# Optimization experiments

Hardware: AMD Instinct MI355X
Metric: run time of the kernel (lower is better)

## Reference

```python
import jax, jax.numpy as jnp
import numpy as np

BS, N, FIN = 128, 320, 1
H1, F1 = 8, 18   # layer-1 heads / hidden
H2, F2 = 4, 46   # layer-2 heads / hidden
D1 = H1 * F1     # 144
D2 = H2 * F2     # 184
FC = (104, 45, 84)
ALPHA = 0.2
NEG = -9e15


def _xavier(key, shape):
    fan_in, fan_out = shape[-2], shape[-1]
    s = 1.414 * np.sqrt(2.0 / (fan_in + fan_out))
    return jax.random.normal(key, shape, dtype=jnp.float32) * s


def setup_inputs() -> dict:
    key = jax.random.key(0)
    ks = jax.random.split(key, 20)
    xnodes = jax.random.normal(ks[0], (BS, N, FIN), dtype=jnp.float32)
    adj = (jax.random.uniform(ks[1], (N, N)) < 0.1).astype(jnp.float32)
    adj = jnp.maximum(adj, jnp.eye(N, dtype=jnp.float32))
    inp = {
        'xnodes': xnodes,
        'adj': adj,
        'W1': _xavier(ks[2], (H1, FIN, F1)),
        'a1': _xavier(ks[3], (H1, 2 * F1)),
        'W2': _xavier(ks[4], (H2, D1, F2)),
        'a2': _xavier(ks[5], (H2, 2 * F2)),
        'p1w': _xavier(ks[6], (D1, 1))[:, 0],
        'p1b': jnp.zeros((), jnp.float32),
        'p2w': _xavier(ks[7], (D2, 1))[:, 0],
        'p2b': jnp.zeros((), jnp.float32),
        'e1w': _xavier(ks[8], (3 * N, FC[0])),
        'e1b': jnp.zeros((FC[0],), jnp.float32),
        'e2w': _xavier(ks[9], (FC[0], FC[1])),
        'e2b': jnp.zeros((FC[1],), jnp.float32),
        'e3w': _xavier(ks[10], (FC[1], FC[2])),
        'e3b': jnp.zeros((FC[2],), jnp.float32),
        'cw': _xavier(ks[11], (FC[2], 1))[:, 0],
        'cb': jnp.zeros((), jnp.float32),
    }
    return inp


def _gat(x, adj_mask, W, a):
    """Multi-head GAT layer (all heads vectorized).
    x: [b,n,fin], W: [h,fin,f], a: [h,2f], adj_mask: [n,n] bool.
    Score e_ij = leakyrelu(a_src.h_i + a_dst.h_j) == concat-matmul of the
    original, without materializing the [b,n,n,2f] tensor.
    """
    h = jnp.einsum('bni,hif->bhnf', x, W)              # [b,h,n,f]
    f = h.shape[-1]
    es = jnp.einsum('bhnf,hf->bhn', h, a[:, :f])       # source term
    ed = jnp.einsum('bhnf,hf->bhn', h, a[:, f:])       # dest term
    e = jax.nn.leaky_relu(es[:, :, :, None] + ed[:, :, None, :], ALPHA)
    e = jnp.where(adj_mask[None, None], e, NEG)
    att = jax.nn.softmax(e, axis=-1)                   # [b,h,n,n]
    hp = jnp.einsum('bhnm,bhmf->bhnf', att, h)
    out = jax.nn.elu(hp)                               # concat=True
    b = out.shape[0]
    return out.transpose(0, 2, 1, 3).reshape(b, out.shape[2], -1)  # [b,n,h*f]


def reference(xnodes, adj, W1, a1, W2, a2, p1w, p1b, p2w, p2b,
              e1w, e1b, e2w, e2b, e3w, e3b, cw, cb):
    mask = adj > 0
    x0 = jnp.mean(xnodes, axis=-1)                     # [b,n]
    x = _gat(xnodes, mask, W1, a1)                     # [b,n,144]
    x1 = x @ p1w + p1b                                 # pool1 -> [b,n]
    x = _gat(x, mask, W2, a2)                          # [b,n,184]
    x2 = x @ p2w + p2b                                 # pool2 -> [b,n]
    x_concat = jnp.concatenate([x0, x1, x2], axis=1)   # [b,3n]
    h = jax.nn.elu(x_concat @ e1w + e1b)
    h = jax.nn.elu(h @ e2w + e2b)
    features = jax.nn.elu(h @ e3w + e3b)               # [b,84]
    hazard = (features @ cw + cb).reshape(-1)          # [b]
    return (x_concat, features, hazard)
```

## Files before the change

### kernel.cpp

```cpp
#include <hip/hip_runtime.h>
#include <hip/hip_bf16.h>
#include <math.h>

#define BS 128
#define NN 320
#define H1 8
#define F1 18
#define H2C 4
#define F2 46
#define FC0 104
#define FC1 45
#define FC2 84
#define LRA 0.2f
#define DEGCAP 96
#define PW 104

typedef __attribute__((ext_vector_type(8))) short bf16x8;
typedef __attribute__((ext_vector_type(4))) float f32x4;

__device__ __forceinline__ float wave_max64(float v) {
    #pragma unroll
    for (int off = 32; off > 0; off >>= 1)
        v = fmaxf(v, __shfl_xor(v, off, 64));
    return v;
}
__device__ __forceinline__ short bfb(float x) {
    __hip_bfloat16 b = __float2bfloat16(x);
    return *(short*)&b;
}

__global__ void k_csr(const float* __restrict__ adj,
                      unsigned short* __restrict__ cols16,
                      unsigned short* __restrict__ colsT16,
                      int4* __restrict__ meta, const float* __restrict__ W1,
                      const float* __restrict__ a1, float* __restrict__ c1s,
                      float* __restrict__ c1d, const float* __restrict__ W2,
                      __hip_bfloat16* __restrict__ Bb) {
    int row = blockIdx.x;
    int lane = threadIdx.x;
    if (row < NN) {
        int base = 0, c96 = 0, c192 = 0, c288 = 0;
        for (int c0 = 0; c0 < NN; c0 += 64) {
            int j = c0 + lane;
            bool p = (j < NN) && (adj[row * NN + j] > 0.f);
            unsigned long long m = __ballot(p);
            if (p) {
                int pos = base + __popcll(m & ((1ull << lane) - 1ull));
                if (pos < DEGCAP) {
                    cols16[row * DEGCAP + pos] = (unsigned short)j;
                    colsT16[pos * NN + row] = (unsigned short)j;
                }
            }
            base += __popcll(m);
            c96  += __popcll(__ballot(p && j < 96));
            c192 += __popcll(__ballot(p && j < 192));
            c288 += __popcll(__ballot(p && j < 288));
        }
        if (base > DEGCAP) base = DEGCAP;
        if (c96 > DEGCAP) c96 = DEGCAP;
        if (c192 > DEGCAP) c192 = DEGCAP;
        if (c288 > DEGCAP) c288 = DEGCAP;
        for (int q = base + lane; q < DEGCAP; q += 64) {
            cols16[row * DEGCAP + q] = 0;
            colsT16[q * NN + row] = 0;
        }
        if (lane == 0) meta[row] = make_int4(c96, c192, c288, base);
    } else if (row == NN) {
        int h = lane;
        if (h < H1) {
            float s = 0.f, d = 0.f;
            for (int f = 0; f < F1; ++f) {
                float w = W1[h * F1 + f];
                s += w * a1[h * 2 * F1 + f];
                d += w * a1[h * 2 * F1 + F1 + f];
            }
            c1s[h] = s;
            c1d[h] = d;
        }
    } else {
        int idx = (row - NN - 1) * 64 + lane;
        int e = idx & 7;
        int t = idx >> 3;
        int n = t % 192, k8 = t / 192;
        int k = k8 * 8 + e, hh = n / 48, f = n - hh * 48;
        float v = (k < 144 && f < 46) ? W2[(hh * 144 + k) * 46 + f] : 0.f;
        Bb[idx] = __float2bfloat16(v);
    }
}

__global__ __launch_bounds__(320) void k_l1(
    const float* __restrict__ xn, const unsigned short* __restrict__ colsT16,
    const int4* __restrict__ meta, const float* __restrict__ W1,
    const float* __restrict__ c1s, const float* __restrict__ c1d,
    const float* __restrict__ p1w, float* __restrict__ sg,
    float* __restrict__ part1) {
    int b = blockIdx.x >> 3, h = blockIdx.x & 7;
    __shared__ float xb[NN];
    __shared__ float w1h[F1], pwl[F1];
    __shared__ float redmax[5], redmin[5];
    int tid = threadIdx.x;
    int wv = tid >> 6, lane = tid & 63;
    float xi = xn[b * NN + tid];
    xb[tid] = xi;
    if (tid < F1) { w1h[tid] = W1[h * F1 + tid]; pwl[tid] = p1w[h * F1 + tid]; }
    int Li = meta[tid].w;
    float mx = wave_max64(xi);
    float mn = -wave_max64(-xi);
    int Lmax = (int)wave_max64((float)Li);
    if (lane == 0) { redmax[wv] = mx; redmin[wv] = mn; }
    __syncthreads();
    float MX = redmax[0], MN = redmin[0];
    #pragma unroll
    for (int q = 1; q < 5; ++q) {
        MX = fmaxf(MX, redmax[q]);
        MN = fminf(MN, redmin[q]);
    }
    float cs = c1s[h], cd = c1d[h];
    float u = xi * cs;
    float mt = u + (cd > 0.f ? cd * MX : cd * MN);
    float m = fmaxf(mt, LRA * mt);
    float num = 0.f, den = 0.f;
    const unsigned short* ct = colsT16 + tid;
    int colv = ct[0];
    for (int j = 0; j < Lmax; ++j) {
        int coln = (j + 1 < Lmax) ? ct[(j + 1) * NN] : 0;
        float xj = xb[colv];
        bool act = j < Li;
        float t = fmaf(xj, cd, u);
        t = fmaxf(t, LRA * t);
        float w = __expf(t - m);
        w = act ? w : 0.f;
        num = fmaf(w, xj, num);
        den += w;
        colv = coln;
    }
    float s = num / den;
    sg[(size_t)(b * 8 + h) * NN + tid] = s;
    float part = 0.f;
    #pragma unroll
    for (int f = 0; f < F1; ++f) {
        float v = s * w1h[f];
        v = v > 0.f ? v : expm1f(v);
        part = fmaf(v, pwl[f], part);
    }
    part1[(size_t)(b * 8 + h) * NN + tid] = part;
}

__global__ __launch_bounds__(256) void k_l2(
    const float* __restrict__ sg, const unsigned short* __restrict__ cols16,
    const int4* __restrict__ meta, const __hip_bfloat16* __restrict__ Bb,
    const float* __restrict__ W1, const float* __restrict__ a2,
    const float* __restrict__ p2w, float* __restrict__ part2) {
    int bh = blockIdx.x;
    int b = bh >> 2, h = bh & 3;
    __shared__ __align__(16) __hip_bfloat16 HT[48][328];
    __shared__ __align__(16) __hip_bfloat16 AsP[4][16][PW];
    __shared__ __align__(16) unsigned short colsW[4][16][DEGCAP];
    __shared__ float sglW[4][8][16];
    __shared__ float esl[NN], edl[NN];
    __shared__ float denW[4][16];
    __shared__ float w1l[8][F1];
    __shared__ float pwl[48], a2e[48], a2d[48];
    __shared__ float Mred[4];
    int tid = threadIdx.x, wv = tid >> 6, lane = tid & 63;
    int lr = lane & 15, lq = lane >> 4;
    if (tid < 48) {
        pwl[tid] = tid < 46 ? p2w[h * F2 + tid] : 0.f;
        a2e[tid] = tid < 46 ? a2[h * 92 + tid] : 0.f;
        a2d[tid] = tid < 46 ? a2[h * 92 + 46 + tid] : 0.f;
    }
    if (tid < 144) {
        int hh = tid / F1, f = tid - hh * F1;
        w1l[hh][f] = W1[hh * F1 + f];
    }
    bf16x8 bq[5][3];
    #pragma unroll
    for (int kc = 0; kc < 5; ++kc)
        #pragma unroll
        for (int t = 0; t < 3; ++t)
            bq[kc][t] = *(const bf16x8*)(Bb +
                (size_t)(((kc * 4 + lq) * 192) + h * 48 + t * 16 + lr) * 8);
    __syncthreads();
    for (int tile = 0; tile < 5; ++tile) {
        int r0 = tile * 64;
        for (int q = lane; q < 128; q += 64) {
            int hh = q >> 4, row = q & 15;
            sglW[wv][hh][row] = sg[(size_t)(b * 8 + hh) * NN + r0 + wv * 16 + row];
        }
        f32x4 acc[3];
        #pragma unroll
        for (int t = 0; t < 3; ++t) acc[t] = (f32x4){0.f, 0.f, 0.f, 0.f};
        #pragma unroll
        for (int sp = 0; sp < 2; ++sp) {
            const int nch = sp ? 2 : 3;
            #pragma unroll
            for (int j = 0; j < nch; ++j) {
                int chunk = (sp ? 12 : 0) + lq + 4 * j;
                int cb = chunk * 8;
                bf16x8 pv;
                #pragma unroll
                for (int e = 0; e < 8; ++e) {
                    unsigned c = cb + e;
                    float v = 0.f;
                    if (c < 144) {
                        unsigned hh = c / 18, f = c - hh * 18;
                        v = sglW[wv][hh][lr] * w1l[hh][f];
                        v = v > 0.f ? v : expm1f(v);
                    }
                    pv[e] = bfb(v);
                }
                *(bf16x8*)&AsP[wv][lr][cb - sp * 96] = pv;
            }
            const int nkc = sp ? 2 : 3;
            #pragma unroll
            for (int kc2 = 0; kc2 < nkc; ++kc2) {
                bf16x8 a = *(const bf16x8*)&AsP[wv][lr][kc2 * 32 + lq * 8];
                int gkc = sp ? 3 + kc2 : kc2;
                #pragma unroll
                for (int t = 0; t < 3; ++t)
                    acc[t] = __builtin_amdgcn_mfma_f32_16x16x32_bf16(
                        a, bq[gkc][t], acc[t], 0, 0, 0);
            }
        }
        int node = r0 + wv * 16 + lq * 4;
        #pragma unroll
        for (int t = 0; t < 3; ++t) {
            short4 s4;
            s4.x = bfb(acc[t][0]); s4.y = bfb(acc[t][1]);
            s4.z = bfb(acc[t][2]); s4.w = bfb(acc[t][3]);
            *(short4*)&HT[t * 16 + lr][node] = s4;
        }
        float esa[4] = {0.f, 0.f, 0.f, 0.f}, eda[4] = {0.f, 0.f, 0.f, 0.f};
        #pragma unroll
        for (int t = 0; t < 3; ++t) {
            float ae = a2e[t * 16 + lr], ad = a2d[t * 16 + lr];
            #pragma unroll
            for (int j = 0; j < 4; ++j) {
                esa[j] = fmaf(acc[t][j], ae, esa[j]);
                eda[j] = fmaf(acc[t][j], ad, eda[j]);
            }
        }
        #pragma unroll
        for (int j = 0; j < 4; ++j) {
            #pragma unroll
            for (int off = 1; off < 16; off <<= 1) {
                esa[j] += __shfl_xor(esa[j], off, 64);
                eda[j] += __shfl_xor(eda[j], off, 64);
            }
        }
        if (lr == 0) {
            #pragma unroll
            for (int j = 0; j < 4; ++j) {
                esl[node + j] = esa[j];
                edl[node + j] = eda[j];
            }
        }
    }
    __syncthreads();
    float edmax = -1e30f;
    for (int i = tid; i < NN; i += 256) edmax = fmaxf(edmax, edl[i]);
    float wm = wave_max64(edmax);
    if (lane == 0) Mred[wv] = wm;
    __syncthreads();
    float M = fmaxf(fmaxf(Mred[0], Mred[1]), fmaxf(Mred[2], Mred[3]));
    for (int tile = 0; tile < 5; ++tile) {
        int r0 = tile * 64;
        for (int q = lane; q < 192; q += 64) {
            int rr = q / 12, c8 = q - rr * 12;
            *(uint4*)&colsW[wv][rr][c8 * 8] =
                *(const uint4*)(cols16 + (size_t)(r0 + wv * 16 + rr) * DEGCAP + c8 * 8);
        }
        int i = r0 + wv * 16 + lr;
        int4 mt = meta[i];
        int sb0 = mt.x, sb1 = mt.y, sb2 = mt.z, sb3 = mt.w;
        float es = esl[i];
        float t0 = es + M;
        float m = fmaxf(t0, LRA * t0);
        f32x4 acc[3];
        #pragma unroll
        for (int t = 0; t < 3; ++t) acc[t] = (f32x4){0.f, 0.f, 0.f, 0.f};
        float dp = 0.f;
        #pragma unroll
        for (int pass = 0; pass < 4; ++pass) {
            for (int q = lane; q < 208; q += 64) {
                int rr = q / 13, cc = q - rr * 13;
                *(uint4*)&AsP[wv][rr][cc * 8] = (uint4){0u, 0u, 0u, 0u};
            }
            int s0 = pass == 0 ? 0 : (pass == 1 ? sb0 : (pass == 2 ? sb1 : sb2));
            int s1 = pass == 0 ? sb0 : (pass == 1 ? sb1 : (pass == 2 ? sb2 : sb3));
            int pofs = pass * 96;
            for (int j = s0 + lq; j < s1; j += 4) {
                int col = colsW[wv][lr][j];
                float t = es + edl[col];
                t = fmaxf(t, LRA * t);
                float w = __expf(t - m);
                dp += w;
                AsP[wv][lr][col - pofs] = __float2bfloat16(w);
            }
            const int nkf = (pass < 3) ? 3 : 1;
            #pragma unroll
            for (int kf = 0; kf < nkf; ++kf) {
                bf16x8 a = *(const bf16x8*)&AsP[wv][lr][kf * 32 + lq * 8];
                #pragma unroll
                for (int t = 0; t < 3; ++t) {
                    bf16x8 bb = *(const bf16x8*)&HT[t * 16 + lr][pofs + kf * 32 + lq * 8];
                    acc[t] = __builtin_amdgcn_mfma_f32_16x16x32_bf16(
                        a, bb, acc[t], 0, 0, 0);
                }
            }
        }
        dp += __shfl_xor(dp, 16, 64);
        dp += __shfl_xor(dp, 32, 64);
        if (lq == 0) denW[wv][lr] = dp;
        float inv[4], part[4];
        #pragma unroll
        for (int j = 0; j < 4; ++j) {
            inv[j] = 1.f / denW[wv][lq * 4 + j];
            part[j] = 0.f;
        }
        #pragma unroll
        for (int t = 0; t < 3; ++t) {
            float pw = pwl[t * 16 + lr];
            #pragma unroll
            for (int j = 0; j < 4; ++j) {
                float v = acc[t][j] * inv[j];
                v = v > 0.f ? v : expm1f(v);
                part[j] = fmaf(v, pw, part[j]);
            }
        }
        #pragma unroll
        for (int j = 0; j < 4; ++j) {
            #pragma unroll
            for (int off = 1; off < 16; off <<= 1)
                part[j] += __shfl_xor(part[j], off, 64);
        }
        if (lr == 0) {
            #pragma unroll
            for (int j = 0; j < 4; ++j)
                part2[(size_t)bh * NN + r0 + wv * 16 + lq * 4 + j] = part[j];
        }
    }
}

__global__ __launch_bounds__(256) void k_head(
    const float* __restrict__ xn, const float* __restrict__ part1,
    const float* __restrict__ part2, const float* __restrict__ p1b,
    const float* __restrict__ p2b, const float* __restrict__ e1w,
    const float* __restrict__ e1b, const float* __restrict__ e2w,
    const float* __restrict__ e2b, const float* __restrict__ e3w,
    const float* __restrict__ e3b, const float* __restrict__ cw,
    const float* __restrict__ cb, float* __restrict__ dout) {
    int b = blockIdx.x;
    int tid = threadIdx.x;
    __shared__ float xc[960];
    __shared__ float e1part[2][FC0];
    __shared__ float h1[FC0];
    __shared__ float hh[FC1];
    __shared__ float ft[FC2];
    for (int t = tid; t < NN; t += 256) {
        float x0 = xn[b * NN + t];
        xc[t] = x0;
        dout[b * 960 + t] = x0;
        float s1 = p1b[0];
        #pragma unroll
        for (int h = 0; h < 8; ++h) s1 += part1[(size_t)(b * 8 + h) * NN + t];
        xc[320 + t] = s1;
        dout[b * 960 + 320 + t] = s1;
        float s2 = p2b[0];
        #pragma unroll
        for (int h = 0; h < 4; ++h) s2 += part2[(size_t)(b * 4 + h) * NN + t];
        xc[640 + t] = s2;
        dout[b * 960 + 640 + t] = s2;
    }
    __syncthreads();
    {
        int half = tid >> 7, o = tid & 127;
        if (o < FC0) {
            float a = 0.f;
            int k0 = half * 480;
            for (int k = k0; k < k0 + 480; ++k)
                a = fmaf(xc[k], e1w[k * FC0 + o], a);
            e1part[half][o] = a;
        }
    }
    __syncthreads();
    if (tid < FC0) {
        float a = e1b[tid] + e1part[0][tid] + e1part[1][tid];
        h1[tid] = a > 0.f ? a : expm1f(a);
    }
    __syncthreads();
    if (tid < FC1) {
        float a = e2b[tid];
        for (int k = 0; k < FC0; ++k) a += h1[k] * e2w[k * FC1 + tid];
        hh[tid] = a > 0.f ? a : expm1f(a);
    }
    __syncthreads();
    if (tid < FC2) {
        float a = e3b[tid];
        for (int k = 0; k < FC1; ++k) a += hh[k] * e3w[k * FC2 + tid];
        a = a > 0.f ? a : expm1f(a);
        ft[tid] = a;
        dout[BS * 960 + b * FC2 + tid] = a;
    }
    __syncthreads();
    if (tid < 64) {
        float v = 0.f;
        for (int t = tid; t < FC2; t += 64) v += ft[t] * cw[t];
        #pragma unroll
        for (int off = 32; off > 0; off >>= 1) v += __shfl_xor(v, off, 64);
        if (tid == 0) dout[BS * 960 + BS * FC2 + b] = v + cb[0];
    }
}

extern "C" void kernel_launch(void* const* d_in, const int* in_sizes, int n_in,
                              void* d_out, int out_size, void* d_ws,
                              size_t ws_size, hipStream_t stream) {
    const float* xn  = (const float*)d_in[0];
    const float* adj = (const float*)d_in[1];
    const float* W1  = (const float*)d_in[2];
    const float* a1  = (const float*)d_in[3];
    const float* W2  = (const float*)d_in[4];
    const float* a2  = (const float*)d_in[5];
    const float* p1w = (const float*)d_in[6];
    const float* p1b = (const float*)d_in[7];
    const float* p2w = (const float*)d_in[8];
    const float* p2b = (const float*)d_in[9];
    const float* e1w = (const float*)d_in[10];
    const float* e1b = (const float*)d_in[11];
    const float* e2w = (const float*)d_in[12];
    const float* e2b = (const float*)d_in[13];
    const float* e3w = (const float*)d_in[14];
    const float* e3b = (const float*)d_in[15];
    const float* cw  = (const float*)d_in[16];
    const float* cb  = (const float*)d_in[17];

    char* ws = (char*)d_ws;
    int4*  meta     = (int4*)ws;
    float* c1s      = (float*)(ws + 5120);
    float* c1d      = (float*)(ws + 5152);
    unsigned short* cols16  = (unsigned short*)(ws + 5248);
    unsigned short* colsT16 = (unsigned short*)(ws + 66688);
    __hip_bfloat16* Bb = (__hip_bfloat16*)(ws + 128128);
    float* sg       = (float*)(ws + 189568);
    float* part1    = (float*)(ws + 1500288);
    float* part2    = (float*)(ws + 2811008);
    float* dout     = (float*)d_out;

    k_csr<<<NN + 1 + 480, 64, 0, stream>>>(adj, cols16, colsT16, meta,
                                           W1, a1, c1s, c1d, W2, Bb);
    k_l1<<<BS * H1, 320, 0, stream>>>(xn, colsT16, meta, W1, c1s, c1d,
                                      p1w, sg, part1);
    k_l2<<<BS * H2C, 256, 0, stream>>>(sg, cols16, meta, Bb, W1, a2, p2w, part2);
    k_head<<<BS, 256, 0, stream>>>(xn, part1, part2, p1b, p2b, e1w, e1b,
                                   e2w, e2b, e3w, e3b, cw, cb, dout);
}
```

Measured before the change: 181.5 us.

## Materialize layer-1 ELU output as bf16 and feed MFMA directly from global

Layer 1 now computes the ELU of each head's output once and stores it as a padded bf16 [batch,node,160] matrix. Layer 2 loads MFMA A fragments directly from that buffer instead of recomputing ELU per element from the per-head scalars in shared memory. expm1f is replaced by __expf-1. This removes redundant transcendental work in layer 2, at the cost of a much larger intermediate buffer, strided stores in layer 1, and reduced precision of ELU near zero.

```diff
diff --git a/kernel.cpp b/kernel.cpp
--- a/kernel.cpp
+++ b/kernel.cpp
@@ -92,7 +92,7 @@
     const float* __restrict__ xn, const unsigned short* __restrict__ colsT16,
     const int4* __restrict__ meta, const float* __restrict__ W1,
     const float* __restrict__ c1s, const float* __restrict__ c1d,
-    const float* __restrict__ p1w, float* __restrict__ sg,
+    const float* __restrict__ p1w, __hip_bfloat16* __restrict__ out1b,
     float* __restrict__ part1) {
     int b = blockIdx.x >> 3, h = blockIdx.x & 7;
     __shared__ float xb[NN];
@@ -135,31 +135,44 @@
         colv = coln;
     }
     float s = num / den;
-    sg[(size_t)(b * 8 + h) * NN + tid] = s;
     float part = 0.f;
+    unsigned od[9];
     #pragma unroll
-    for (int f = 0; f < F1; ++f) {
-        float v = s * w1h[f];
-        v = v > 0.f ? v : expm1f(v);
-        part = fmaf(v, pwl[f], part);
+    for (int f = 0; f < F1; f += 2) {
+        float v0 = s * w1h[f];
+        v0 = v0 > 0.f ? v0 : __expf(v0) - 1.f;
+        float v1 = s * w1h[f + 1];
+        v1 = v1 > 0.f ? v1 : __expf(v1) - 1.f;
+        part = fmaf(v0, pwl[f], part);
+        part = fmaf(v1, pwl[f + 1], part);
+        od[f >> 1] = (unsigned)(unsigned short)bfb(v0) |
+                     ((unsigned)(unsigned short)bfb(v1) << 16);
+    }
+    __hip_bfloat16* rowp = out1b + (size_t)(b * NN + tid) * 160;
+    unsigned* dst = (unsigned*)(rowp + h * F1);
+    #pragma unroll
+    for (int q = 0; q < 9; ++q) dst[q] = od[q];
+    if (h == 0) {
+        uint4 z = (uint4){0u, 0u, 0u, 0u};
+        *(uint4*)(rowp + 144) = z;
+        *(uint4*)(rowp + 152) = z;
     }
     part1[(size_t)(b * 8 + h) * NN + tid] = part;
 }
 
 __global__ __launch_bounds__(256) void k_l2(
-    const float* __restrict__ sg, const unsigned short* __restrict__ cols16,
+    const __hip_bfloat16* __restrict__ out1b,
+    const unsigned short* __restrict__ cols16,
     const int4* __restrict__ meta, const __hip_bfloat16* __restrict__ Bb,
-    const float* __restrict__ W1, const float* __restrict__ a2,
-    const float* __restrict__ p2w, float* __restrict__ part2) {
+    const float* __restrict__ a2, const float* __restrict__ p2w,
+    float* __restrict__ part2) {
     int bh = blockIdx.x;
     int b = bh >> 2, h = bh & 3;
     __shared__ __align__(16) __hip_bfloat16 HT[48][328];
     __shared__ __align__(16) __hip_bfloat16 AsP[4][16][PW];
     __shared__ __align__(16) unsigned short colsW[4][16][DEGCAP];
-    __shared__ float sglW[4][8][16];
     __shared__ float esl[NN], edl[NN];
     __shared__ float denW[4][16];
-    __shared__ float w1l[8][F1];
     __shared__ float pwl[48], a2e[48], a2d[48];
     __shared__ float Mred[4];
     int tid = threadIdx.x, wv = tid >> 6, lane = tid & 63;
@@ -169,10 +182,6 @@
         a2e[tid] = tid < 46 ? a2[h * 92 + tid] : 0.f;
         a2d[tid] = tid < 46 ? a2[h * 92 + 46 + tid] : 0.f;
     }
-    if (tid < 144) {
-        int hh = tid / F1, f = tid - hh * F1;
-        w1l[hh][f] = W1[hh * F1 + f];
-    }
     bf16x8 bq[5][3];
     #pragma unroll
     for (int kc = 0; kc < 5; ++kc)
@@ -181,46 +190,20 @@
             bq[kc][t] = *(const bf16x8*)(Bb +
                 (size_t)(((kc * 4 + lq) * 192) + h * 48 + t * 16 + lr) * 8);
     __syncthreads();
+    const __hip_bfloat16* Ag = out1b + (size_t)b * NN * 160;
     for (int tile = 0; tile < 5; ++tile) {
         int r0 = tile * 64;
-        for (int q = lane; q < 128; q += 64) {
-            int hh = q >> 4, row = q & 15;
-            sglW[wv][hh][row] = sg[(size_t)(b * 8 + hh) * NN + r0 + wv * 16 + row];
-        }
+        const __hip_bfloat16* arow = Ag + (size_t)(r0 + wv * 16 + lr) * 160 + lq * 8;
         f32x4 acc[3];
         #pragma unroll
         for (int t = 0; t < 3; ++t) acc[t] = (f32x4){0.f, 0.f, 0.f, 0.f};
         #pragma unroll
-        for (int sp = 0; sp < 2; ++sp) {
-            const int nch = sp ? 2 : 3;
-            #pragma unroll
-            for (int j = 0; j < nch; ++j) {
-                int chunk = (sp ? 12 : 0) + lq + 4 * j;
-                int cb = chunk * 8;
-                bf16x8 pv;
-                #pragma unroll
-                for (int e = 0; e < 8; ++e) {
-                    unsigned c = cb + e;
-                    float v = 0.f;
-                    if (c < 144) {
-                        unsigned hh = c / 18, f = c - hh * 18;
-                        v = sglW[wv][hh][lr] * w1l[hh][f];
-                        v = v > 0.f ? v : expm1f(v);
-                    }
-                    pv[e] = bfb(v);
-                }
-                *(bf16x8*)&AsP[wv][lr][cb - sp * 96] = pv;
-            }
-            const int nkc = sp ? 2 : 3;
-            #pragma unroll
-            for (int kc2 = 0; kc2 < nkc; ++kc2) {
-                bf16x8 a = *(const bf16x8*)&AsP[wv][lr][kc2 * 32 + lq * 8];
-                int gkc = sp ? 3 + kc2 : kc2;
-                #pragma unroll
-                for (int t = 0; t < 3; ++t)
-                    acc[t] = __builtin_amdgcn_mfma_f32_16x16x32_bf16(
-                        a, bq[gkc][t], acc[t], 0, 0, 0);
-            }
+        for (int kc = 0; kc < 5; ++kc) {
+            bf16x8 a = *(const bf16x8*)(arow + kc * 32);
+            #pragma unroll
+            for (int t = 0; t < 3; ++t)
+                acc[t] = __builtin_amdgcn_mfma_f32_16x16x32_bf16(
+                    a, bq[kc][t], acc[t], 0, 0, 0);
         }
         int node = r0 + wv * 16 + lq * 4;
         #pragma unroll
@@ -324,7 +307,7 @@
             #pragma unroll
             for (int j = 0; j < 4; ++j) {
                 float v = acc[t][j] * inv[j];
-                v = v > 0.f ? v : expm1f(v);
+                v = v > 0.f ? v : __expf(v) - 1.f;
                 part[j] = fmaf(v, pw, part[j]);
             }
         }
@@ -441,16 +424,16 @@
     unsigned short* cols16  = (unsigned short*)(ws + 5248);
     unsigned short* colsT16 = (unsigned short*)(ws + 66688);
     __hip_bfloat16* Bb = (__hip_bfloat16*)(ws + 128128);
-    float* sg       = (float*)(ws + 189568);
-    float* part1    = (float*)(ws + 1500288);
-    float* part2    = (float*)(ws + 2811008);
+    __hip_bfloat16* out1b = (__hip_bfloat16*)(ws + 189568);
+    float* part1    = (float*)(ws + 13296768);
+    float* part2    = (float*)(ws + 14607488);
     float* dout     = (float*)d_out;
 
     k_csr<<<NN + 1 + 480, 64, 0, stream>>>(adj, cols16, colsT16, meta,
                                            W1, a1, c1s, c1d, W2, Bb);
     k_l1<<<BS * H1, 320, 0, stream>>>(xn, colsT16, meta, W1, c1s, c1d,
-                                      p1w, sg, part1);
-    k_l2<<<BS * H2C, 256, 0, stream>>>(sg, cols16, meta, Bb, W1, a2, p2w, part2);
+                                      p1w, out1b, part1);
+    k_l2<<<BS * H2C, 256, 0, stream>>>(out1b, cols16, meta, Bb, a2, p2w, part2);
     k_head<<<BS, 256, 0, stream>>>(xn, part1, part2, p1b, p2b, e1w, e1b,
                                    e2w, e2b, e3w, e3b, cw, cb, dout);
 }
```

Result: faster. 165.2 us (-9.0%).
